# Kernel optimization log

Measured on AMD Instinct MI355X. Metric: run time of the kernel, lower is better.

The kernel has to match this reference:

```python
import jax, jax.numpy as jnp
import numpy as np

ROUTINGS = 3

def squash(s, axis=-1):
    mag_sq = jnp.sum(s * s, axis=axis, keepdims=True)
    mag = jnp.sqrt(mag_sq)
    return mag_sq / (1.0 + mag_sq) * (s / (mag + 1e-8))

def setup_inputs() -> dict:
    key = jax.random.key(0)
    k1, k2 = jax.random.split(key)
    B, I, Din, O, Dout = 256, 1152, 8, 10, 16
    x = jax.random.normal(k1, (B, I, Din), dtype=jnp.float32)
    weight = 0.01 * jax.random.normal(k2, (O, I, Dout, Din), dtype=jnp.float32)
    return {"x": x, "weight": weight}

def reference(x, weight):
    # x: [B, I, Din]; weight: [O, I, Dout, Din]
    # x_hat: [B, O, I, Dout]
    x_hat = jnp.einsum('oidc,bic->boid', weight, x)
    x_hat_det = jax.lax.stop_gradient(x_hat)
    B, O, I, _ = x_hat.shape
    b = jnp.zeros((B, O, I), dtype=x_hat.dtype)
    outputs = None
    for i in range(ROUTINGS):
        c = jax.nn.softmax(b, axis=1)  # softmax over output capsules
        if i == ROUTINGS - 1:
            outputs = squash(jnp.sum(c[:, :, :, None] * x_hat, axis=2, keepdims=True))
        else:
            outputs = squash(jnp.sum(c[:, :, :, None] * x_hat_det, axis=2, keepdims=True))
            b = b + jnp.sum(outputs * x_hat_det, axis=-1)
    return jnp.squeeze(outputs, axis=2)  # [B, O, Dout]
```

## Files before the change

### kernel.cpp

```cpp
#include <hip/hip_runtime.h>

#define BB   256
#define II   1152
#define OO   10
#define DOUT 16

using h2 = __fp16 __attribute__((ext_vector_type(2)));
using h4 = __fp16 __attribute__((ext_vector_type(4)));
using h8 = __fp16 __attribute__((ext_vector_type(8)));
#define H2V(v, a, b) __builtin_shufflevector((v), (v), (a), (b))
#define FD(a, b, c)  __builtin_amdgcn_fdot2((a), (b), (c), false)

typedef __attribute__((address_space(3))) uint32_t lds_u32_t;
typedef __attribute__((address_space(1))) const uint32_t glb_u32_t;

__device__ __forceinline__ void dma16(const __fp16* g, __fp16* l) {
  __builtin_amdgcn_global_load_lds((glb_u32_t*)g, (lds_u32_t*)l, 16, 0, 0);
}

__device__ __forceinline__ float dpp_add_xor1(float v) {
  int r = __builtin_amdgcn_mov_dpp(__float_as_int(v), 0xB1, 0xF, 0xF, true);
  return v + __int_as_float(r);
}
__device__ __forceinline__ float dpp_add_xor2(float v) {
  int r = __builtin_amdgcn_mov_dpp(__float_as_int(v), 0x4E, 0xF, 0xF, true);
  return v + __int_as_float(r);
}
__device__ __forceinline__ float swz_add_xor4(float v) {
  int r = __builtin_amdgcn_ds_swizzle(__float_as_int(v), 0x101F);
  return v + __int_as_float(r);
}

__device__ __forceinline__ void squash_pair(float v0, float v1,
                                            float& o0, float& o1) {
  float sq = v0 * v0 + v1 * v1;
  sq += __shfl_xor(sq, 1);
  sq += __shfl_xor(sq, 2);
  sq += __shfl_xor(sq, 4);
  const float mag = sqrtf(sq);
  const float t1  = sq / (1.f + sq);
  o0 = t1 * (v0 / (mag + 1e-8f));
  o1 = t1 * (v1 / (mag + 1e-8f));
}

__global__ __launch_bounds__(256) void convert_kernel(
    const float* __restrict__ x, const float* __restrict__ w,
    __fp16* __restrict__ x16, __fp16* __restrict__ w16)
{
  const int bid = blockIdx.x;
  if (bid < 2880) {
    const int t = bid * 256 + threadIdx.x;
    const int e = t & 63;
    const int r = t >> 6;
    const int o = r / II;
    const int i = r - o * II;
    const float2 v2 = *(const float2*)(w + (size_t)r * 128 + e * 2);
    *(h2*)(w16 + ((size_t)i * 12 + o) * 128 + e * 2) =
        __builtin_amdgcn_cvt_pkrtz(v2.x, v2.y);
  } else {
    const size_t t = (size_t)(bid - 2880) * 256 + threadIdx.x;
    const float4 v4 = *(const float4*)(x + t * 4);
    const h2 a = __builtin_amdgcn_cvt_pkrtz(v4.x, v4.y);
    const h2 c = __builtin_amdgcn_cvt_pkrtz(v4.z, v4.w);
    *(h4*)(x16 + t * 4) = __builtin_shufflevector(a, c, 0, 1, 2, 3);
  }
}

template<int K>
__global__ __launch_bounds__(256, 4) void pass_kernel(
    const __fp16* __restrict__ x16,
    const __fp16* __restrict__ w16,
    const float* __restrict__ r0,
    const float* __restrict__ r1,
    float* __restrict__ plane)
{
  const int tid  = threadIdx.x;
  const int lane = tid & 63;
  const int wv   = tid >> 6;
  const int dsub = lane & 7;
  const int bl   = lane >> 3;
  const int icg  = blockIdx.x & 31;
  const int bg   = blockIdx.x >> 5;
  const int b    = bg * 8 + bl;
  const int i0   = (icg * 4 + wv) * 9;

  __shared__ __fp16 wt[4][3 * 1536];
  __fp16* const wbuf = wt[wv];

  float Vr[OO][2];
  if (K >= 1) {
#pragma unroll
    for (int o = 0; o < OO; ++o) {
      const float2 a = *(const float2*)(r0 + ((size_t)b * OO + o) * DOUT + dsub * 2);
      float v0, v1;
      squash_pair(a.x, a.y, v0, v1);
      if (K == 2) {
        const float2 c = *(const float2*)(r1 + ((size_t)b * OO + o) * DOUT + dsub * 2);
        float u0, u1;
        squash_pair(c.x, c.y, u0, u1);
        v0 += u0; v1 += u1;
      }
      Vr[o][0] = v0; Vr[o][1] = v1;
    }
  }

  float s[OO][2];
#pragma unroll
  for (int o = 0; o < OO; ++o) { s[o][0] = 0.f; s[o][1] = 0.f; }

  #define STAGE(i_, ofs_)                                                      \
    {                                                                          \
      const __fp16* gp = w16 + (size_t)(i_) * 1536 + lane * 8;                 \
      dma16(gp,        wbuf + (ofs_));                                         \
      dma16(gp + 512,  wbuf + (ofs_) + 512);                                   \
      dma16(gp + 1024, wbuf + (ofs_) + 1024);                                  \
    }

  const __fp16* xrow = x16 + ((size_t)b * II + i0) * 8;
  STAGE(i0, 0)
  h8 xq = *(const h8*)(xrow);
  asm volatile("" ::: "memory");
  STAGE(i0 + 1, 1536)
  h8 xn = *(const h8*)(xrow + 8);

  int cur = 0;
#pragma unroll 1
  for (int ii = 0; ii < 9; ++ii) {
    asm volatile("s_waitcnt vmcnt(4)" ::: "memory");
    __builtin_amdgcn_sched_barrier(0);

    const __fp16* wtb = wbuf + cur * 1536;
    const h2 xq0 = H2V(xq, 0, 1), xq1 = H2V(xq, 2, 3);
    const h2 xq2 = H2V(xq, 4, 5), xq3 = H2V(xq, 6, 7);

    float xh[OO][2];
    float t[OO];
#pragma unroll
    for (int half = 0; half < 2; ++half) {
      h8 wz[10];
      const __fp16* base = wtb + half * 640 + dsub * 16;
#pragma unroll
      for (int g = 0; g < 5; ++g) {
        wz[2 * g]     = *(const h8*)(base + g * 128);
        wz[2 * g + 1] = *(const h8*)(base + g * 128 + 8);
      }
      __builtin_amdgcn_sched_barrier(0);
#pragma unroll
      for (int g = 0; g < 5; ++g) {
        const int o = half * 5 + g;
        xh[o][0] = FD(H2V(wz[2*g], 0, 1), xq0, FD(H2V(wz[2*g], 2, 3), xq1,
                   FD(H2V(wz[2*g], 4, 5), xq2, FD(H2V(wz[2*g], 6, 7), xq3, 0.f))));
        xh[o][1] = FD(H2V(wz[2*g+1], 0, 1), xq0, FD(H2V(wz[2*g+1], 2, 3), xq1,
                   FD(H2V(wz[2*g+1], 4, 5), xq2, FD(H2V(wz[2*g+1], 6, 7), xq3, 0.f))));
        if (K >= 1)
          t[o] = Vr[o][0] * xh[o][0] + Vr[o][1] * xh[o][1];
      }
    }

    if (K == 0) {
#pragma unroll
      for (int o = 0; o < OO; ++o) { s[o][0] += xh[o][0]; s[o][1] += xh[o][1]; }
    } else {
#pragma unroll
      for (int o = 0; o < OO; ++o) {
        t[o] = dpp_add_xor1(t[o]);
        t[o] = dpp_add_xor2(t[o]);
        t[o] = swz_add_xor4(t[o]);
      }
      float sum = 0.f;
#pragma unroll
      for (int o = 0; o < OO; ++o) { t[o] = __expf(t[o]); sum += t[o]; }
      const float inv = __builtin_amdgcn_rcpf(sum);
#pragma unroll
      for (int o = 0; o < OO; ++o) {
        const float c = t[o] * inv;
        s[o][0] += c * xh[o][0];
        s[o][1] += c * xh[o][1];
      }
    }

    const int inx = (ii < 7) ? (i0 + ii + 2) : (i0 + 8);
    int nbuf = cur - 1; if (nbuf < 0) nbuf += 3;
    STAGE(inx, nbuf * 1536)
    xq = xn;
    xn = *(const h8*)(x16 + ((size_t)b * II + inx) * 8);

    cur += 1; if (cur == 3) cur = 0;
  }
  #undef STAGE

  if (K == 0) {
#pragma unroll
    for (int o = 0; o < OO; ++o) { s[o][0] *= 0.1f; s[o][1] *= 0.1f; }
  }

  asm volatile("s_waitcnt vmcnt(0)" ::: "memory");
  if (wv != 0) {
    float* rr = (float*)&wt[wv][0] + bl * 168;
#pragma unroll
    for (int o = 0; o < OO; ++o)
      *(float2*)&rr[o * 16 + dsub * 2] = make_float2(s[o][0], s[o][1]);
  }
  __syncthreads();
  if (wv == 0) {
    float* outp = plane + (size_t)b * (OO * DOUT);
#pragma unroll
    for (int o = 0; o < OO; ++o) {
      float a0 = s[o][0], a1 = s[o][1];
#pragma unroll
      for (int r = 1; r < 4; ++r) {
        const float2 v2 = *(const float2*)((const float*)&wt[r][0] +
                                           bl * 168 + o * 16 + dsub * 2);
        a0 += v2.x; a1 += v2.y;
      }
      unsafeAtomicAdd(&outp[o * 16 + dsub * 2],     a0);
      unsafeAtomicAdd(&outp[o * 16 + dsub * 2 + 1], a1);
    }
  }
}

__global__ __launch_bounds__(256) void final_kernel(
    const float* __restrict__ plane,
    float* __restrict__ out)
{
  const int idx = blockIdx.x * 256 + threadIdx.x;
  const float s = plane[idx];

  float sq = s * s;
  sq += __shfl_xor(sq, 1);
  sq += __shfl_xor(sq, 2);
  sq += __shfl_xor(sq, 4);
  sq += __shfl_xor(sq, 8);
  const float mag = sqrtf(sq);
  out[idx] = sq / (1.f + sq) * (s / (mag + 1e-8f));
}

extern "C" void kernel_launch(void* const* d_in, const int* in_sizes, int n_in,
                              void* d_out, int out_size, void* d_ws, size_t ws_size,
                              hipStream_t stream) {
  const float* x = (const float*)d_in[0];
  const float* w = (const float*)d_in[1];
  float* outp = (float*)d_out;

  const size_t P = (size_t)BB * OO * DOUT;
  float* s0 = (float*)d_ws;
  float* s1 = s0 + P;
  float* s2 = s1 + P;
  __fp16* x16 = (__fp16*)(s2 + P);
  __fp16* w16 = x16 + (size_t)BB * II * 8;

  hipMemsetAsync(s0, 0, 3 * P * sizeof(float), stream);
  convert_kernel<<<5184, 256, 0, stream>>>(x, w, x16, w16);

  const int pg = 1024;
  const int fg = (int)(P / 256);

  pass_kernel<0><<<pg, 256, 0, stream>>>(x16, w16, nullptr, nullptr, s0);
  pass_kernel<1><<<pg, 256, 0, stream>>>(x16, w16, s0, nullptr, s1);
  pass_kernel<2><<<pg, 256, 0, stream>>>(x16, w16, s0, s1, s2);
  final_kernel<<<fg, 256, 0, stream>>>(s2, outp);
}
```

Measured before the change: 148.9 us.

## Materialize x_hat in fp16 once and reuse it in the routing passes

New measurement: 140.7 us. 5.5% less time.

```diff
diff --git a/kernel.cpp b/kernel.cpp
--- a/kernel.cpp
+++ b/kernel.cpp
@@ -66,10 +66,128 @@
   }
 }
 
-template<int K>
-__global__ __launch_bounds__(256, 4) void pass_kernel(
+__global__ __launch_bounds__(256, 4) void einsum_kernel(
     const __fp16* __restrict__ x16,
     const __fp16* __restrict__ w16,
+    __fp16* __restrict__ xh16,
+    float* __restrict__ plane)
+{
+  const int tid  = threadIdx.x;
+  const int lane = tid & 63;
+  const int wv   = tid >> 6;
+  const int dsub = lane & 7;
+  const int bl   = lane >> 3;
+  const int icg  = blockIdx.x & 31;
+  const int bg   = blockIdx.x >> 5;
+  const int b    = bg * 8 + bl;
+  const int i0   = (icg * 4 + wv) * 9;
+  const int lb   = b * 16 + dsub * 2;
+
+  __shared__ __fp16 wt[4][3 * 1536];
+  __fp16* const wbuf = wt[wv];
+
+  float s[OO][2];
+#pragma unroll
+  for (int o = 0; o < OO; ++o) { s[o][0] = 0.f; s[o][1] = 0.f; }
+
+  #define STAGE(i_, ofs_)                                                      \
+    {                                                                          \
+      const __fp16* gp = w16 + (size_t)(i_) * 1536 + lane * 8;                 \
+      dma16(gp,        wbuf + (ofs_));                                         \
+      dma16(gp + 512,  wbuf + (ofs_) + 512);                                   \
+      dma16(gp + 1024, wbuf + (ofs_) + 1024);                                  \
+    }
+
+  const __fp16* xrow = x16 + ((size_t)b * II + i0) * 8;
+  STAGE(i0, 0)
+  h8 xq = *(const h8*)(xrow);
+  asm volatile("" ::: "memory");
+  STAGE(i0 + 1, 1536)
+  h8 xn = *(const h8*)(xrow + 8);
+
+  int cur = 0;
+#pragma unroll 1
+  for (int ii = 0; ii < 9; ++ii) {
+    asm volatile("s_waitcnt vmcnt(4)" ::: "memory");
+    __builtin_amdgcn_sched_barrier(0);
+
+    const int i = i0 + ii;
+    const __fp16* wtb = wbuf + cur * 1536;
+    const h2 xq0 = H2V(xq, 0, 1), xq1 = H2V(xq, 2, 3);
+    const h2 xq2 = H2V(xq, 4, 5), xq3 = H2V(xq, 6, 7);
+
+    float xh[OO][2];
+#pragma unroll
+    for (int half = 0; half < 2; ++half) {
+      h8 wz[10];
+      const __fp16* base = wtb + half * 640 + dsub * 16;
+#pragma unroll
+      for (int g = 0; g < 5; ++g) {
+        wz[2 * g]     = *(const h8*)(base + g * 128);
+        wz[2 * g + 1] = *(const h8*)(base + g * 128 + 8);
+      }
+      __builtin_amdgcn_sched_barrier(0);
+#pragma unroll
+      for (int g = 0; g < 5; ++g) {
+        const int o = half * 5 + g;
+        xh[o][0] = FD(H2V(wz[2*g], 0, 1), xq0, FD(H2V(wz[2*g], 2, 3), xq1,
+                   FD(H2V(wz[2*g], 4, 5), xq2, FD(H2V(wz[2*g], 6, 7), xq3, 0.f))));
+        xh[o][1] = FD(H2V(wz[2*g+1], 0, 1), xq0, FD(H2V(wz[2*g+1], 2, 3), xq1,
+                   FD(H2V(wz[2*g+1], 4, 5), xq2, FD(H2V(wz[2*g+1], 6, 7), xq3, 0.f))));
+      }
+    }
+
+#pragma unroll
+    for (int o = 0; o < OO; ++o) { s[o][0] += xh[o][0]; s[o][1] += xh[o][1]; }
+
+    {
+      __fp16* op = xh16 + (size_t)i * (OO * 4096) + lb;
+#pragma unroll
+      for (int o = 0; o < OO; ++o)
+        *(h2*)(op + o * 4096) = __builtin_amdgcn_cvt_pkrtz(xh[o][0], xh[o][1]);
+    }
+
+    const int inx = (ii < 7) ? (i0 + ii + 2) : (i0 + 8);
+    int nbuf = cur - 1; if (nbuf < 0) nbuf += 3;
+    STAGE(inx, nbuf * 1536)
+    xq = xn;
+    xn = *(const h8*)(x16 + ((size_t)b * II + inx) * 8);
+
+    cur += 1; if (cur == 3) cur = 0;
+  }
+  #undef STAGE
+
+#pragma unroll
+  for (int o = 0; o < OO; ++o) { s[o][0] *= 0.1f; s[o][1] *= 0.1f; }
+
+  asm volatile("s_waitcnt vmcnt(0)" ::: "memory");
+  if (wv != 0) {
+    float* rr = (float*)&wt[wv][0] + bl * 168;
+#pragma unroll
+    for (int o = 0; o < OO; ++o)
+      *(float2*)&rr[o * 16 + dsub * 2] = make_float2(s[o][0], s[o][1]);
+  }
+  __syncthreads();
+  if (wv == 0) {
+    float* outp = plane + (size_t)b * (OO * DOUT);
+#pragma unroll
+    for (int o = 0; o < OO; ++o) {
+      float a0 = s[o][0], a1 = s[o][1];
+#pragma unroll
+      for (int r = 1; r < 4; ++r) {
+        const float2 v2 = *(const float2*)((const float*)&wt[r][0] +
+                                           bl * 168 + o * 16 + dsub * 2);
+        a0 += v2.x; a1 += v2.y;
+      }
+      unsafeAtomicAdd(&outp[o * 16 + dsub * 2],     a0);
+      unsafeAtomicAdd(&outp[o * 16 + dsub * 2 + 1], a1);
+    }
+  }
+}
+
+template<int K>
+__global__ __launch_bounds__(256, 4) void route_kernel(
+    const __fp16* __restrict__ xh16,
     const float* __restrict__ r0,
     const float* __restrict__ r1,
     float* __restrict__ plane)
@@ -83,120 +201,66 @@
   const int bg   = blockIdx.x >> 5;
   const int b    = bg * 8 + bl;
   const int i0   = (icg * 4 + wv) * 9;
-
-  __shared__ __fp16 wt[4][3 * 1536];
-  __fp16* const wbuf = wt[wv];
+  const int lb   = b * 16 + dsub * 2;
+
+  __shared__ float red[4][8 * 168];
 
   float Vr[OO][2];
-  if (K >= 1) {
-#pragma unroll
-    for (int o = 0; o < OO; ++o) {
-      const float2 a = *(const float2*)(r0 + ((size_t)b * OO + o) * DOUT + dsub * 2);
-      float v0, v1;
-      squash_pair(a.x, a.y, v0, v1);
-      if (K == 2) {
-        const float2 c = *(const float2*)(r1 + ((size_t)b * OO + o) * DOUT + dsub * 2);
-        float u0, u1;
-        squash_pair(c.x, c.y, u0, u1);
-        v0 += u0; v1 += u1;
-      }
-      Vr[o][0] = v0; Vr[o][1] = v1;
-    }
+#pragma unroll
+  for (int o = 0; o < OO; ++o) {
+    const float2 a = *(const float2*)(r0 + ((size_t)b * OO + o) * DOUT + dsub * 2);
+    float v0, v1;
+    squash_pair(a.x, a.y, v0, v1);
+    if (K == 2) {
+      const float2 c = *(const float2*)(r1 + ((size_t)b * OO + o) * DOUT + dsub * 2);
+      float u0, u1;
+      squash_pair(c.x, c.y, u0, u1);
+      v0 += u0; v1 += u1;
+    }
+    Vr[o][0] = v0; Vr[o][1] = v1;
   }
 
   float s[OO][2];
 #pragma unroll
   for (int o = 0; o < OO; ++o) { s[o][0] = 0.f; s[o][1] = 0.f; }
 
-  #define STAGE(i_, ofs_)                                                      \
-    {                                                                          \
-      const __fp16* gp = w16 + (size_t)(i_) * 1536 + lane * 8;                 \
-      dma16(gp,        wbuf + (ofs_));                                         \
-      dma16(gp + 512,  wbuf + (ofs_) + 512);                                   \
-      dma16(gp + 1024, wbuf + (ofs_) + 1024);                                  \
-    }
-
-  const __fp16* xrow = x16 + ((size_t)b * II + i0) * 8;
-  STAGE(i0, 0)
-  h8 xq = *(const h8*)(xrow);
-  asm volatile("" ::: "memory");
-  STAGE(i0 + 1, 1536)
-  h8 xn = *(const h8*)(xrow + 8);
-
-  int cur = 0;
 #pragma unroll 1
   for (int ii = 0; ii < 9; ++ii) {
-    asm volatile("s_waitcnt vmcnt(4)" ::: "memory");
-    __builtin_amdgcn_sched_barrier(0);
-
-    const __fp16* wtb = wbuf + cur * 1536;
-    const h2 xq0 = H2V(xq, 0, 1), xq1 = H2V(xq, 2, 3);
-    const h2 xq2 = H2V(xq, 4, 5), xq3 = H2V(xq, 6, 7);
+    const int i = i0 + ii;
+    const __fp16* bp = xh16 + (size_t)i * (OO * 4096) + lb;
+
+    h2 xv[OO];
+#pragma unroll
+    for (int o = 0; o < OO; ++o) xv[o] = *(const h2*)(bp + o * 4096);
 
     float xh[OO][2];
     float t[OO];
 #pragma unroll
-    for (int half = 0; half < 2; ++half) {
-      h8 wz[10];
-      const __fp16* base = wtb + half * 640 + dsub * 16;
-#pragma unroll
-      for (int g = 0; g < 5; ++g) {
-        wz[2 * g]     = *(const h8*)(base + g * 128);
-        wz[2 * g + 1] = *(const h8*)(base + g * 128 + 8);
-      }
-      __builtin_amdgcn_sched_barrier(0);
-#pragma unroll
-      for (int g = 0; g < 5; ++g) {
-        const int o = half * 5 + g;
-        xh[o][0] = FD(H2V(wz[2*g], 0, 1), xq0, FD(H2V(wz[2*g], 2, 3), xq1,
-                   FD(H2V(wz[2*g], 4, 5), xq2, FD(H2V(wz[2*g], 6, 7), xq3, 0.f))));
-        xh[o][1] = FD(H2V(wz[2*g+1], 0, 1), xq0, FD(H2V(wz[2*g+1], 2, 3), xq1,
-                   FD(H2V(wz[2*g+1], 4, 5), xq2, FD(H2V(wz[2*g+1], 6, 7), xq3, 0.f))));
-        if (K >= 1)
-          t[o] = Vr[o][0] * xh[o][0] + Vr[o][1] * xh[o][1];
-      }
-    }
-
-    if (K == 0) {
-#pragma unroll
-      for (int o = 0; o < OO; ++o) { s[o][0] += xh[o][0]; s[o][1] += xh[o][1]; }
-    } else {
-#pragma unroll
-      for (int o = 0; o < OO; ++o) {
-        t[o] = dpp_add_xor1(t[o]);
-        t[o] = dpp_add_xor2(t[o]);
-        t[o] = swz_add_xor4(t[o]);
-      }
-      float sum = 0.f;
-#pragma unroll
-      for (int o = 0; o < OO; ++o) { t[o] = __expf(t[o]); sum += t[o]; }
-      const float inv = __builtin_amdgcn_rcpf(sum);
-#pragma unroll
-      for (int o = 0; o < OO; ++o) {
-        const float c = t[o] * inv;
-        s[o][0] += c * xh[o][0];
-        s[o][1] += c * xh[o][1];
-      }
-    }
-
-    const int inx = (ii < 7) ? (i0 + ii + 2) : (i0 + 8);
-    int nbuf = cur - 1; if (nbuf < 0) nbuf += 3;
-    STAGE(inx, nbuf * 1536)
-    xq = xn;
-    xn = *(const h8*)(x16 + ((size_t)b * II + inx) * 8);
-
-    cur += 1; if (cur == 3) cur = 0;
-  }
-  #undef STAGE
-
-  if (K == 0) {
-#pragma unroll
-    for (int o = 0; o < OO; ++o) { s[o][0] *= 0.1f; s[o][1] *= 0.1f; }
-  }
-
-  asm volatile("s_waitcnt vmcnt(0)" ::: "memory");
+    for (int o = 0; o < OO; ++o) {
+      xh[o][0] = (float)xv[o][0];
+      xh[o][1] = (float)xv[o][1];
+      t[o] = Vr[o][0] * xh[o][0] + Vr[o][1] * xh[o][1];
+    }
+#pragma unroll
+    for (int o = 0; o < OO; ++o) {
+      t[o] = dpp_add_xor1(t[o]);
+      t[o] = dpp_add_xor2(t[o]);
+      t[o] = swz_add_xor4(t[o]);
+    }
+    float sum = 0.f;
+#pragma unroll
+    for (int o = 0; o < OO; ++o) { t[o] = __expf(t[o]); sum += t[o]; }
+    const float inv = __builtin_amdgcn_rcpf(sum);
+#pragma unroll
+    for (int o = 0; o < OO; ++o) {
+      const float c = t[o] * inv;
+      s[o][0] += c * xh[o][0];
+      s[o][1] += c * xh[o][1];
+    }
+  }
+
   if (wv != 0) {
-    float* rr = (float*)&wt[wv][0] + bl * 168;
+    float* rr = red[wv] + bl * 168;
 #pragma unroll
     for (int o = 0; o < OO; ++o)
       *(float2*)&rr[o * 16 + dsub * 2] = make_float2(s[o][0], s[o][1]);
@@ -209,8 +273,7 @@
       float a0 = s[o][0], a1 = s[o][1];
 #pragma unroll
       for (int r = 1; r < 4; ++r) {
-        const float2 v2 = *(const float2*)((const float*)&wt[r][0] +
-                                           bl * 168 + o * 16 + dsub * 2);
+        const float2 v2 = *(const float2*)(red[r] + bl * 168 + o * 16 + dsub * 2);
         a0 += v2.x; a1 += v2.y;
       }
       unsafeAtomicAdd(&outp[o * 16 + dsub * 2],     a0);
@@ -248,6 +311,7 @@
   float* s2 = s1 + P;
   __fp16* x16 = (__fp16*)(s2 + P);
   __fp16* w16 = x16 + (size_t)BB * II * 8;
+  __fp16* xh16 = w16 + (size_t)II * 12 * 128;
 
   hipMemsetAsync(s0, 0, 3 * P * sizeof(float), stream);
   convert_kernel<<<5184, 256, 0, stream>>>(x, w, x16, w16);
@@ -255,8 +319,8 @@
   const int pg = 1024;
   const int fg = (int)(P / 256);
 
-  pass_kernel<0><<<pg, 256, 0, stream>>>(x16, w16, nullptr, nullptr, s0);
-  pass_kernel<1><<<pg, 256, 0, stream>>>(x16, w16, s0, nullptr, s1);
-  pass_kernel<2><<<pg, 256, 0, stream>>>(x16, w16, s0, s1, s2);
+  einsum_kernel<<<pg, 256, 0, stream>>>(x16, w16, xh16, s0);
+  route_kernel<1><<<pg, 256, 0, stream>>>(xh16, s0, nullptr, s1);
+  route_kernel<2><<<pg, 256, 0, stream>>>(xh16, s0, s1, s2);
   final_kernel<<<fg, 256, 0, stream>>>(s2, outp);
 }
```
